# Kernel tuning notes

Measured on AMD Instinct MI355X. Metric: run time of the kernel, lower is better.

Reference implementation:

```python
import jax, jax.numpy as jnp
import numpy as np

B, S, TEXT_DIM, VISION_DIM, HIDDEN, HEADS = 4, 2048, 768, 768, 512, 8
HEAD_DIM = HIDDEN // HEADS


def setup_inputs() -> dict:
    key = jax.random.key(0)
    ks = jax.random.split(key, 9)
    s_in = 1.0 / np.sqrt(TEXT_DIM)
    s_h = 1.0 / np.sqrt(HIDDEN)
    return {
        "text_embeds": jax.random.normal(ks[0], (B, S, TEXT_DIM), dtype=jnp.float32),
        "Wq": jax.random.uniform(ks[1], (TEXT_DIM, HIDDEN), jnp.float32, -s_in, s_in),
        "bq": jax.random.uniform(ks[2], (HIDDEN,), jnp.float32, -s_in, s_in),
        "Wk": jax.random.uniform(ks[3], (TEXT_DIM, HIDDEN), jnp.float32, -s_in, s_in),
        "bk": jax.random.uniform(ks[4], (HIDDEN,), jnp.float32, -s_in, s_in),
        "Wv": jax.random.uniform(ks[5], (TEXT_DIM, HIDDEN), jnp.float32, -s_in, s_in),
        "bv": jax.random.uniform(ks[6], (HIDDEN,), jnp.float32, -s_in, s_in),
        "Wo": jax.random.uniform(ks[7], (HIDDEN, VISION_DIM), jnp.float32, -s_h, s_h),
        "bo": jax.random.uniform(ks[8], (VISION_DIM,), jnp.float32, -s_h, s_h),
    }


def reference(text_embeds, Wq, bq, Wk, bk, Wv, bv, Wo, bo):
    b, s, _ = text_embeds.shape
    # QKV projections -> [b, heads, s, head_dim]
    def proj(W, bias):
        y = jnp.einsum("bsd,dh->bsh", text_embeds, W) + bias
        return y.reshape(b, s, HEADS, HEAD_DIM).transpose(0, 2, 1, 3)
    q, k, v = proj(Wq, bq), proj(Wk, bk), proj(Wv, bv)
    scores = jnp.einsum("bhqd,bhkd->bhqk", q, k) / np.sqrt(HEAD_DIM).astype(np.float32)
    weights = jax.nn.softmax(scores, axis=-1)
    attended = jnp.einsum("bhqk,bhkd->bhqd", weights, v)
    attended = attended.transpose(0, 2, 1, 3).reshape(b, s, HIDDEN)
    out = jnp.einsum("bsh,hv->bsv", attended, Wo) + bo
    return jnp.squeeze(out, axis=1) if out.shape[1] == 1 else out
```

## Files before the change

kernel.cpp:

```cpp
#include <hip/hip_runtime.h>
#include <hip/hip_bf16.h>

#define BATCH 4
#define SEQ 2048
#define TDIM 768
#define VDIM 768
#define HID 512
#define NHEADS 8
#define HDIM 64
#define MROWS (BATCH * SEQ)
#define NQKV (3 * HID)

typedef unsigned short ushort_t;
typedef __attribute__((ext_vector_type(8))) short short8;
typedef __attribute__((ext_vector_type(4))) short short4v;
typedef __attribute__((ext_vector_type(4))) float floatx4;

#define QSCALE 0.18033688011112042f

__device__ __forceinline__ ushort_t bf16_rne(float f) {
    unsigned int u = __float_as_uint(f);
    u = (u + 0x7fffu + ((u >> 16) & 1u)) >> 16;
    return (ushort_t)u;
}

__device__ __forceinline__ float bf16_to_f(ushort_t v) {
    return __uint_as_float(((unsigned)v) << 16);
}

__device__ __forceinline__ void async16(const ushort_t* g, ushort_t* l) {
    __builtin_amdgcn_global_load_lds(
        (const __attribute__((address_space(1))) unsigned int*)g,
        (__attribute__((address_space(3))) unsigned int*)l, 16, 0, 0);
}

__global__ __launch_bounds__(256) void conv_x(const float* __restrict__ X,
                                              ushort_t* __restrict__ Xb)
{
    const int i = (blockIdx.x * 256 + threadIdx.x) * 4;
    const floatx4 v = *(const floatx4*)(X + i);
    short4v o;
#pragma unroll
    for (int j = 0; j < 4; ++j) o[j] = (short)bf16_rne(v[j]);
    *(short4v*)(Xb + i) = o;
}

__global__ __launch_bounds__(256) void transp_w(
    const float* __restrict__ Wq, const float* __restrict__ Wk,
    const float* __restrict__ Wv, const float* __restrict__ Wo,
    ushort_t* __restrict__ Wqkvt, ushort_t* __restrict__ Wot)
{
    __shared__ float tile[32][33];
    const int z = blockIdx.z;
    const float* src;
    ushort_t* dst;
    int R, C;
    if (z < 3) {
        src = (z == 0) ? Wq : (z == 1) ? Wk : Wv;
        dst = Wqkvt + (size_t)z * HID * TDIM;
        R = TDIM; C = HID;
    } else {
        src = Wo; dst = Wot; R = HID; C = VDIM;
    }
    const int tx = threadIdx.x & 31, ty = threadIdx.x >> 5;
    const int c0 = blockIdx.x * 32, r0 = blockIdx.y * 32;
    if (c0 >= C || r0 >= R) return;
#pragma unroll
    for (int i = 0; i < 4; ++i)
        tile[ty + i * 8][tx] = src[(size_t)(r0 + ty + i * 8) * C + c0 + tx];
    __syncthreads();
#pragma unroll
    for (int i = 0; i < 4; ++i)
        dst[(size_t)(c0 + ty + i * 8) * R + r0 + tx] = bf16_rne(tile[tx][ty + i * 8]);
}

template<int KD, bool SWAPPED>
__device__ __forceinline__ void gemm128(
    const ushort_t* __restrict__ A, const ushort_t* __restrict__ Bt,
    int m0, int n0, ushort_t* As, ushort_t* Bs, floatx4 (&acc)[4][4])
{
    const int tid  = threadIdx.x;
    const int lane = tid & 63;
    const int w    = tid >> 6;
    const int l15  = lane & 15;
    const int quad = lane >> 4;
    const int wrow = w >> 1;
    const int wcol = w & 1;

    const int srow = lane >> 3;
    const int scol = (lane & 7) * 8;

    const ushort_t* ga = A  + (size_t)(m0 + w * 32 + srow) * KD + scol;
    const ushort_t* gb = Bt + (size_t)(n0 + w * 32 + srow) * KD + scol;
    ushort_t* la = As + (w * 32) * 64;
    ushort_t* lb = Bs + (w * 32) * 64;

    for (int kt = 0; kt < KD; kt += 64) {
#pragma unroll
        for (int i = 0; i < 4; ++i) {
            async16(ga + (size_t)(i * 8) * KD + kt, la + i * 8 * 64);
            async16(gb + (size_t)(i * 8) * KD + kt, lb + i * 8 * 64);
        }
        __syncthreads();
#pragma unroll
        for (int half = 0; half < 2; ++half) {
            const int kk = half * 32 + quad * 8;
            short8 af[4], bf[4];
#pragma unroll
            for (int t = 0; t < 4; ++t) {
                af[t] = *(const short8*)&As[(wrow * 64 + t * 16 + l15) * 64 + kk];
                bf[t] = *(const short8*)&Bs[(wcol * 64 + t * 16 + l15) * 64 + kk];
            }
#pragma unroll
            for (int mi = 0; mi < 4; ++mi)
#pragma unroll
                for (int ni = 0; ni < 4; ++ni) {
                    if (SWAPPED)
                        acc[mi][ni] = __builtin_amdgcn_mfma_f32_16x16x32_bf16(
                            bf[ni], af[mi], acc[mi][ni], 0, 0, 0);
                    else
                        acc[mi][ni] = __builtin_amdgcn_mfma_f32_16x16x32_bf16(
                            af[mi], bf[ni], acc[mi][ni], 0, 0, 0);
                }
        }
        __syncthreads();
    }
}

__global__ __launch_bounds__(256) void qkv_gemm_mfma(
    const ushort_t* __restrict__ Xb, const ushort_t* __restrict__ Wt,
    const float* __restrict__ bq, const float* __restrict__ bk,
    const float* __restrict__ bv,
    ushort_t* __restrict__ Q, ushort_t* __restrict__ K, ushort_t* __restrict__ V)
{
    __shared__ __align__(16) ushort_t As[128 * 64];
    __shared__ __align__(16) ushort_t Bs[128 * 64];

    const int bx = blockIdx.x;
    const int m0 = blockIdx.y * 128;
    const int n0 = bx * 128;
    const int which = bx >> 2;
    const bool isV = (which == 2);

    floatx4 acc[4][4];
#pragma unroll
    for (int i = 0; i < 4; ++i)
#pragma unroll
        for (int j = 0; j < 4; ++j) acc[i][j] = (floatx4)0.0f;

    if (isV) gemm128<TDIM, false>(Xb, Wt, m0, n0, As, Bs, acc);
    else     gemm128<TDIM, true >(Xb, Wt, m0, n0, As, Bs, acc);

    const int lane = threadIdx.x & 63;
    const int w    = threadIdx.x >> 6;
    const int l15  = lane & 15;
    const int quad = lane >> 4;
    const int wrow = w >> 1;
    const int wcol = w & 1;

    if (!isV) {
        const float* bias = (which == 0) ? bq : bk;
        const float scale = (which == 0) ? QSCALE : 1.0f;
        ushort_t* Out = (which == 0) ? Q : K;
#pragma unroll
        for (int mi = 0; mi < 4; ++mi) {
            const int m = m0 + wrow * 64 + mi * 16 + l15;
            const int b = m >> 11;
            const int s = m & 2047;
#pragma unroll
            for (int ni = 0; ni < 4; ++ni) {
                const int c = (n0 - which * HID) + wcol * 64 + ni * 16 + quad * 4;
                const int h = c >> 6;
                const int d0 = c & 63;
                const floatx4 b4 = *(const floatx4*)(bias + c);
                short4v pk;
#pragma unroll
                for (int r = 0; r < 4; ++r)
                    pk[r] = (short)bf16_rne((acc[mi][ni][r] + b4[r]) * scale);
                *(short4v*)&Out[((size_t)(b * NHEADS + h) * SEQ + s) * HDIM + d0] = pk;
            }
        }
    } else {
#pragma unroll
        for (int ni = 0; ni < 4; ++ni) {
            const int c = (n0 - 2 * HID) + wcol * 64 + ni * 16 + l15;
            const int h = c >> 6;
            const int d = c & 63;
            const float b1 = bv[c];
#pragma unroll
            for (int mi = 0; mi < 4; ++mi) {
                const int mb = m0 + wrow * 64 + mi * 16 + quad * 4;
                const int b = mb >> 11;
                const int s0 = mb & 2047;
                short4v pk;
#pragma unroll
                for (int r = 0; r < 4; ++r)
                    pk[r] = (short)bf16_rne(acc[mi][ni][r] + b1);
                *(short4v*)&V[((size_t)(b * NHEADS + h) * HDIM + d) * SEQ + s0] = pk;
            }
        }
    }
}

__global__ __launch_bounds__(512) void flash_attn_mfma(
    const ushort_t* __restrict__ Q, const ushort_t* __restrict__ K,
    const ushort_t* __restrict__ Vt, ushort_t* __restrict__ Opart,
    float* __restrict__ Lpart)
{
    __shared__ __align__(16) ushort_t lds[32768];

    const int tid  = threadIdx.x;
    const int lane = tid & 63;
    const int w    = tid >> 6;
    const int l15  = lane & 15;
    const int quad = lane >> 4;
    const int key  = l15 & 7;

    const int bh = blockIdx.x;
    const int b  = bh >> 3;
    const int h  = bh & 7;
    const int q0 = blockIdx.y * 256;
    const int z  = blockIdx.z;
    const int kk0 = z * (SEQ / 2);

    const ushort_t* Qb = Q  + (size_t)bh * SEQ * HDIM;
    const ushort_t* Kb = K  + (size_t)bh * SEQ * HDIM + (size_t)kk0 * HDIM;
    const ushort_t* Vb = Vt + (size_t)bh * HDIM * SEQ + kk0;

    short8 qfA0, qfA1, qfB0, qfB1;
    {
        const ushort_t* qa = Qb + (size_t)(q0 + w * 32 + l15) * HDIM + quad * 8;
        qfA0 = *(const short8*)(qa);
        qfA1 = *(const short8*)(qa + 32);
        qfB0 = *(const short8*)(qa + 16 * HDIM);
        qfB1 = *(const short8*)(qa + 16 * HDIM + 32);
    }

    float lA = 0.f, lB = 0.f;
    floatx4 ofA[4], ofB[4];
#pragma unroll
    for (int t = 0; t < 4; ++t) { ofA[t] = (floatx4)0.0f; ofB[t] = (floatx4)0.0f; }

    const int srow = tid >> 3;
    const int sg   = tid & 7;
    const ushort_t* gK = Kb + (size_t)srow * HDIM + sg * 8;
    const ushort_t* gV = Vb + (size_t)srow * SEQ + sg * 8;
    const int sofs = srow * 64 + (sg ^ (srow & 7)) * 8;

    ushort_t* Pw = lds + 16384 + w * 2048;

    short8 kr = *(const short8*)(gK);
    short8 vr = *(const short8*)(gV);

    for (int it = 0; it < 16; ++it) {
        const int buf = it & 1;
        *(short8*)&lds[buf * 4096 + sofs]        = kr;
        *(short8*)&lds[8192 + buf * 4096 + sofs] = vr;
        __syncthreads();

        if (it < 15) {
            kr = *(const short8*)(gK + (size_t)(it + 1) * 64 * HDIM);
            vr = *(const short8*)(gV + (it + 1) * 64);
        }

        floatx4 saccA[4], saccB[4];
#pragma unroll
        for (int t = 0; t < 4; ++t) {
            const int kb = buf * 4096 + (t * 16 + l15) * 64;
            const short8 kf0 = *(const short8*)&lds[kb + (quad ^ key) * 8];
            const short8 kf1 = *(const short8*)&lds[kb + ((quad + 4) ^ key) * 8];
            floatx4 a = (floatx4)0.0f, bb = (floatx4)0.0f;
            a  = __builtin_amdgcn_mfma_f32_16x16x32_bf16(kf0, qfA0, a, 0, 0, 0);
            a  = __builtin_amdgcn_mfma_f32_16x16x32_bf16(kf1, qfA1, a, 0, 0, 0);
            bb = __builtin_amdgcn_mfma_f32_16x16x32_bf16(kf0, qfB0, bb, 0, 0, 0);
            bb = __builtin_amdgcn_mfma_f32_16x16x32_bf16(kf1, qfB1, bb, 0, 0, 0);
            saccA[t] = a;
            saccB[t] = bb;
        }

        float rsA = 0.f, rsB = 0.f;
#pragma unroll
        for (int t = 0; t < 4; ++t) {
            float pa[4], pb[4];
#pragma unroll
            for (int r = 0; r < 4; ++r) {
                pa[r] = exp2f(saccA[t][r]); rsA += pa[r];
                pb[r] = exp2f(saccB[t][r]); rsB += pb[r];
            }
            const int pofs = ((2 * t + (quad >> 1)) ^ key) * 8 + (quad & 1) * 4;
            {
                const unsigned u0 = __float_as_uint(pa[0]) + 0x8000u;
                const unsigned u1 = __float_as_uint(pa[1]) + 0x8000u;
                const unsigned u2 = __float_as_uint(pa[2]) + 0x8000u;
                const unsigned u3 = __float_as_uint(pa[3]) + 0x8000u;
                const unsigned lo = __builtin_amdgcn_perm(u1, u0, 0x07060302u);
                const unsigned hi = __builtin_amdgcn_perm(u3, u2, 0x07060302u);
                *(unsigned long long*)&Pw[l15 * 64 + pofs] =
                    ((unsigned long long)hi << 32) | lo;
            }
            {
                const unsigned u0 = __float_as_uint(pb[0]) + 0x8000u;
                const unsigned u1 = __float_as_uint(pb[1]) + 0x8000u;
                const unsigned u2 = __float_as_uint(pb[2]) + 0x8000u;
                const unsigned u3 = __float_as_uint(pb[3]) + 0x8000u;
                const unsigned lo = __builtin_amdgcn_perm(u1, u0, 0x07060302u);
                const unsigned hi = __builtin_amdgcn_perm(u3, u2, 0x07060302u);
                *(unsigned long long*)&Pw[(16 + l15) * 64 + pofs] =
                    ((unsigned long long)hi << 32) | lo;
            }
        }
        lA += rsA;
        lB += rsB;
        asm volatile("s_waitcnt lgkmcnt(0)" ::: "memory");

        const short8 pfA0 = *(const short8*)&Pw[l15 * 64 + (quad ^ key) * 8];
        const short8 pfA1 = *(const short8*)&Pw[l15 * 64 + ((quad + 4) ^ key) * 8];
        const short8 pfB0 = *(const short8*)&Pw[(16 + l15) * 64 + (quad ^ key) * 8];
        const short8 pfB1 = *(const short8*)&Pw[(16 + l15) * 64 + ((quad + 4) ^ key) * 8];

#pragma unroll
        for (int t = 0; t < 4; ++t) {
            const int vb2 = 8192 + buf * 4096 + (t * 16 + l15) * 64;
            const short8 vf0 = *(const short8*)&lds[vb2 + (quad ^ key) * 8];
            const short8 vf1 = *(const short8*)&lds[vb2 + ((quad + 4) ^ key) * 8];
            ofA[t] = __builtin_amdgcn_mfma_f32_16x16x32_bf16(vf0, pfA0, ofA[t], 0, 0, 0);
            ofA[t] = __builtin_amdgcn_mfma_f32_16x16x32_bf16(vf1, pfA1, ofA[t], 0, 0, 0);
            ofB[t] = __builtin_amdgcn_mfma_f32_16x16x32_bf16(vf0, pfB0, ofB[t], 0, 0, 0);
            ofB[t] = __builtin_amdgcn_mfma_f32_16x16x32_bf16(vf1, pfB1, ofB[t], 0, 0, 0);
        }
    }

    lA += __shfl_xor(lA, 16); lA += __shfl_xor(lA, 32);
    lB += __shfl_xor(lB, 16); lB += __shfl_xor(lB, 32);

    const int sA = q0 + w * 32 + l15;
    ushort_t* arowA = Opart + (size_t)z * MROWS * HID
                    + ((size_t)(b * SEQ + sA)) * HID + h * HDIM;
    ushort_t* arowB = arowA + (size_t)16 * HID;
#pragma unroll
    for (int t = 0; t < 4; ++t) {
        short4v pkA, pkB;
#pragma unroll
        for (int r = 0; r < 4; ++r) {
            pkA[r] = (short)bf16_rne(ofA[t][r]);
            pkB[r] = (short)bf16_rne(ofB[t][r]);
        }
        *(short4v*)&arowA[t * 16 + quad * 4] = pkA;
        *(short4v*)&arowB[t * 16 + quad * 4] = pkB;
    }
    if (quad == 0) {
        Lpart[(size_t)(z * 32 + bh) * SEQ + sA]      = lA;
        Lpart[(size_t)(z * 32 + bh) * SEQ + sA + 16] = lB;
    }
}

__global__ __launch_bounds__(256) void combine_halves(
    const ushort_t* __restrict__ Opart, const float* __restrict__ Lpart,
    ushort_t* __restrict__ Att)
{
    const int idx = blockIdx.x * 256 + threadIdx.x;
    const int m  = idx >> 6;
    const int c0 = (idx & 63) * 8;
    const int b = m >> 11;
    const int s = m & 2047;
    const int h = c0 >> 6;
    const int bh = b * 8 + h;

    const float l = Lpart[(size_t)bh * SEQ + s] +
                    Lpart[(size_t)(32 + bh) * SEQ + s];
    const float inv = 1.f / l;

    const short8 o0 = *(const short8*)&Opart[(size_t)m * HID + c0];
    const short8 o1 = *(const short8*)&Opart[(size_t)MROWS * HID + (size_t)m * HID + c0];
    short8 o;
#pragma unroll
    for (int j = 0; j < 8; ++j) {
        const float f = (bf16_to_f((ushort_t)o0[j]) + bf16_to_f((ushort_t)o1[j])) * inv;
        o[j] = (short)bf16_rne(f);
    }
    *(short8*)&Att[(size_t)m * HID + c0] = o;
}

__global__ __launch_bounds__(256) void out_gemm_mfma(
    const ushort_t* __restrict__ Attb, const ushort_t* __restrict__ Wot,
    const float* __restrict__ bo, float* __restrict__ Y)
{
    __shared__ __align__(16) ushort_t As[128 * 64];
    __shared__ __align__(16) ushort_t Bs[128 * 64];

    const int m0 = blockIdx.y * 128;
    const int n0 = blockIdx.x * 128;

    floatx4 acc[4][4];
#pragma unroll
    for (int i = 0; i < 4; ++i)
#pragma unroll
        for (int j = 0; j < 4; ++j) acc[i][j] = (floatx4)0.0f;

    gemm128<HID, true>(Attb, Wot, m0, n0, As, Bs, acc);

    const int lane = threadIdx.x & 63;
    const int w    = threadIdx.x >> 6;
    const int l15  = lane & 15;
    const int quad = lane >> 4;
    const int wrow = w >> 1;
    const int wcol = w & 1;

#pragma unroll
    for (int mi = 0; mi < 4; ++mi) {
        const int m = m0 + wrow * 64 + mi * 16 + l15;
#pragma unroll
        for (int ni = 0; ni < 4; ++ni) {
            const int nb = n0 + wcol * 64 + ni * 16 + quad * 4;
            const floatx4 b4 = *(const floatx4*)(bo + nb);
            floatx4 o;
#pragma unroll
            for (int r = 0; r < 4; ++r) o[r] = acc[mi][ni][r] + b4[r];
            *(floatx4*)&Y[(size_t)m * VDIM + nb] = o;
        }
    }
}

extern "C" void kernel_launch(void* const* d_in, const int* in_sizes, int n_in,
                              void* d_out, int out_size, void* d_ws, size_t ws_size,
                              hipStream_t stream)
{
    const float* text = (const float*)d_in[0];
    const float* Wq = (const float*)d_in[1];
    const float* bq = (const float*)d_in[2];
    const float* Wk = (const float*)d_in[3];
    const float* bk = (const float*)d_in[4];
    const float* Wv = (const float*)d_in[5];
    const float* bv = (const float*)d_in[6];
    const float* Wo = (const float*)d_in[7];
    const float* bo = (const float*)d_in[8];
    float* out = (float*)d_out;

    ushort_t* Xb    = (ushort_t*)d_ws;
    ushort_t* Wqkvt = Xb + (size_t)MROWS * TDIM;
    ushort_t* Wot   = Wqkvt + (size_t)NQKV * TDIM;
    ushort_t* Qw    = Wot + (size_t)VDIM * HID;
    ushort_t* Kw    = Qw + (size_t)MROWS * HID;
    ushort_t* Vtw   = Kw + (size_t)MROWS * HID;
    ushort_t* Opart = Vtw + (size_t)MROWS * HID;
    float*    Lpart = (float*)(Opart + (size_t)2 * MROWS * HID);
    ushort_t* Attb  = Xb;

    conv_x<<<dim3(MROWS * TDIM / 1024), 256, 0, stream>>>(text, Xb);
    transp_w<<<dim3(24, 24, 4), 256, 0, stream>>>(Wq, Wk, Wv, Wo, Wqkvt, Wot);
    qkv_gemm_mfma<<<dim3(12, 64), 256, 0, stream>>>(Xb, Wqkvt, bq, bk, bv, Qw, Kw, Vtw);
    flash_attn_mfma<<<dim3(32, 8, 2), 512, 0, stream>>>(Qw, Kw, Vtw, Opart, Lpart);
    combine_halves<<<dim3(MROWS * HID / 8 / 256), 256, 0, stream>>>(Opart, Lpart, Attb);
    out_gemm_mfma<<<dim3(6, 64), 256, 0, stream>>>(Attb, Wot, bo, out);
}
```

Before: 214.4 us.

## Fuse split-KV combine into output projection GEMM and merge prep kernels

Merges the input conversion and weight transpose into one prep launch, and folds the split-attention combine (sum of two partial outputs divided by the summed softmax denominators) into the A-tile load of a new output-projection GEMM using 128x64 tiles. This removes two kernel launches and the write and reread of the intermediate attention buffer. In exchange, each of the 12 column blocks re-reads both partial outputs and recomputes the normalisation. The new GEMM loads synchronously with no async pipelining and rounds with a simpler add-0x8000 scheme.

```diff
diff --git a/kernel.cpp b/kernel.cpp
--- a/kernel.cpp
+++ b/kernel.cpp
@@ -15,6 +15,7 @@
 typedef __attribute__((ext_vector_type(8))) short short8;
 typedef __attribute__((ext_vector_type(4))) short short4v;
 typedef __attribute__((ext_vector_type(4))) float floatx4;
+typedef __attribute__((ext_vector_type(4))) unsigned int uint4v;
 
 #define QSCALE 0.18033688011112042f
 
@@ -34,24 +35,29 @@
         (__attribute__((address_space(3))) unsigned int*)l, 16, 0, 0);
 }
 
-__global__ __launch_bounds__(256) void conv_x(const float* __restrict__ X,
-                                              ushort_t* __restrict__ Xb)
-{
-    const int i = (blockIdx.x * 256 + threadIdx.x) * 4;
-    const floatx4 v = *(const floatx4*)(X + i);
-    short4v o;
-#pragma unroll
-    for (int j = 0; j < 4; ++j) o[j] = (short)bf16_rne(v[j]);
-    *(short4v*)(Xb + i) = o;
-}
-
-__global__ __launch_bounds__(256) void transp_w(
+__global__ __launch_bounds__(256) void prep(
+    const float* __restrict__ X, ushort_t* __restrict__ Xb,
     const float* __restrict__ Wq, const float* __restrict__ Wk,
     const float* __restrict__ Wv, const float* __restrict__ Wo,
     ushort_t* __restrict__ Wqkvt, ushort_t* __restrict__ Wot)
 {
     __shared__ float tile[32][33];
-    const int z = blockIdx.z;
+    const int bx = blockIdx.x;
+    if (bx < 6144) {
+        const int i = (bx * 256 + threadIdx.x) * 4;
+        const floatx4 v = *(const floatx4*)(X + i);
+        short4v o;
+#pragma unroll
+        for (int j = 0; j < 4; ++j) o[j] = (short)bf16_rne(v[j]);
+        *(short4v*)(Xb + i) = o;
+        return;
+    }
+    const int t = bx - 6144;
+    const int z = t / 576;
+    const int rem = t % 576;
+    const int bxx = rem % 24;
+    const int byy = rem / 24;
+
     const float* src;
     ushort_t* dst;
     int R, C;
@@ -63,7 +69,7 @@
         src = Wo; dst = Wot; R = HID; C = VDIM;
     }
     const int tx = threadIdx.x & 31, ty = threadIdx.x >> 5;
-    const int c0 = blockIdx.x * 32, r0 = blockIdx.y * 32;
+    const int c0 = bxx * 32, r0 = byy * 32;
     if (c0 >= C || r0 >= R) return;
 #pragma unroll
     for (int i = 0; i < 4; ++i)
@@ -354,68 +360,108 @@
     }
 }
 
-__global__ __launch_bounds__(256) void combine_halves(
+__global__ __launch_bounds__(256) void out_proj_fused(
     const ushort_t* __restrict__ Opart, const float* __restrict__ Lpart,
-    ushort_t* __restrict__ Att)
-{
-    const int idx = blockIdx.x * 256 + threadIdx.x;
-    const int m  = idx >> 6;
-    const int c0 = (idx & 63) * 8;
-    const int b = m >> 11;
-    const int s = m & 2047;
-    const int h = c0 >> 6;
-    const int bh = b * 8 + h;
-
-    const float l = Lpart[(size_t)bh * SEQ + s] +
-                    Lpart[(size_t)(32 + bh) * SEQ + s];
-    const float inv = 1.f / l;
-
-    const short8 o0 = *(const short8*)&Opart[(size_t)m * HID + c0];
-    const short8 o1 = *(const short8*)&Opart[(size_t)MROWS * HID + (size_t)m * HID + c0];
-    short8 o;
-#pragma unroll
-    for (int j = 0; j < 8; ++j) {
-        const float f = (bf16_to_f((ushort_t)o0[j]) + bf16_to_f((ushort_t)o1[j])) * inv;
-        o[j] = (short)bf16_rne(f);
-    }
-    *(short8*)&Att[(size_t)m * HID + c0] = o;
-}
-
-__global__ __launch_bounds__(256) void out_gemm_mfma(
-    const ushort_t* __restrict__ Attb, const ushort_t* __restrict__ Wot,
-    const float* __restrict__ bo, float* __restrict__ Y)
+    const ushort_t* __restrict__ Wot, const float* __restrict__ bo,
+    float* __restrict__ Y)
 {
     __shared__ __align__(16) ushort_t As[128 * 64];
-    __shared__ __align__(16) ushort_t Bs[128 * 64];
-
-    const int m0 = blockIdx.y * 128;
-    const int n0 = blockIdx.x * 128;
-
-    floatx4 acc[4][4];
-#pragma unroll
-    for (int i = 0; i < 4; ++i)
-#pragma unroll
-        for (int j = 0; j < 4; ++j) acc[i][j] = (floatx4)0.0f;
-
-    gemm128<HID, true>(Attb, Wot, m0, n0, As, Bs, acc);
-
-    const int lane = threadIdx.x & 63;
-    const int w    = threadIdx.x >> 6;
+    __shared__ __align__(16) ushort_t Bs[64 * 64];
+
+    const int tid  = threadIdx.x;
+    const int lane = tid & 63;
+    const int w    = tid >> 6;
     const int l15  = lane & 15;
     const int quad = lane >> 4;
-    const int wrow = w >> 1;
-    const int wcol = w & 1;
-
-#pragma unroll
-    for (int mi = 0; mi < 4; ++mi) {
-        const int m = m0 + wrow * 64 + mi * 16 + l15;
-#pragma unroll
-        for (int ni = 0; ni < 4; ++ni) {
-            const int nb = n0 + wcol * 64 + ni * 16 + quad * 4;
+    const int key  = l15 & 7;
+
+    const int n0 = blockIdx.x * 64;
+    const int m0 = blockIdx.y * 128;
+
+    const int srow = tid >> 1;
+    const int scol = (tid & 1) * 32;
+    const int am   = m0 + srow;
+    const int ab   = am >> 11;
+    const int as   = am & 2047;
+    const ushort_t* gO0 = Opart + (size_t)am * HID + scol;
+    const ushort_t* gO1 = gO0 + (size_t)MROWS * HID;
+    const int sk = srow & 7;
+
+    const int brow = tid >> 3;
+    const int bg   = tid & 7;
+    const ushort_t* gB = Wot + (size_t)(n0 + brow) * HID + bg * 8;
+
+    floatx4 acc[2][4];
+#pragma unroll
+    for (int i = 0; i < 2; ++i)
+#pragma unroll
+        for (int j = 0; j < 4; ++j) acc[i][j] = (floatx4)0.0f;
+
+    for (int kt = 0; kt < HID; kt += 64) {
+        const int h = kt >> 6;
+        const int bh = ab * 8 + h;
+        const float l = Lpart[(size_t)bh * SEQ + as] +
+                        Lpart[(size_t)(32 + bh) * SEQ + as];
+        const float inv = 1.f / l;
+        if (kt) __syncthreads();
+#pragma unroll
+        for (int seg = 0; seg < 4; ++seg) {
+            const short8 o0 = *(const short8*)(gO0 + h * 64 + seg * 8);
+            const short8 o1 = *(const short8*)(gO1 + h * 64 + seg * 8);
+            uint4v v;
+#pragma unroll
+            for (int p = 0; p < 4; ++p) {
+                const float f0 = (bf16_to_f((ushort_t)o0[2 * p]) +
+                                  bf16_to_f((ushort_t)o1[2 * p])) * inv;
+                const float f1 = (bf16_to_f((ushort_t)o0[2 * p + 1]) +
+                                  bf16_to_f((ushort_t)o1[2 * p + 1])) * inv;
+                const unsigned u0 = __float_as_uint(f0) + 0x8000u;
+                const unsigned u1 = __float_as_uint(f1) + 0x8000u;
+                v[p] = __builtin_amdgcn_perm(u1, u0, 0x07060302u);
+            }
+            const int g = (scol >> 3) + seg;
+            *(uint4v*)&As[srow * 64 + (g ^ sk) * 8] = v;
+        }
+        {
+            const short8 b0 = *(const short8*)(gB + kt);
+            const short8 b1 = *(const short8*)(gB + (size_t)32 * HID + kt);
+            *(short8*)&Bs[brow * 64 + (bg ^ (brow & 7)) * 8] = b0;
+            *(short8*)&Bs[(brow + 32) * 64 + (bg ^ (brow & 7)) * 8] = b1;
+        }
+        __syncthreads();
+
+#pragma unroll
+        for (int half = 0; half < 2; ++half) {
+            short8 af[2], bf[4];
+#pragma unroll
+            for (int t = 0; t < 2; ++t) {
+                const int row = w * 32 + t * 16 + l15;
+                af[t] = *(const short8*)&As[row * 64 + (((half * 4) + quad) ^ key) * 8];
+            }
+#pragma unroll
+            for (int n = 0; n < 4; ++n) {
+                const int row = n * 16 + l15;
+                bf[n] = *(const short8*)&Bs[row * 64 + (((half * 4) + quad) ^ key) * 8];
+            }
+#pragma unroll
+            for (int t = 0; t < 2; ++t)
+#pragma unroll
+                for (int n = 0; n < 4; ++n)
+                    acc[t][n] = __builtin_amdgcn_mfma_f32_16x16x32_bf16(
+                        bf[n], af[t], acc[t][n], 0, 0, 0);
+        }
+    }
+
+#pragma unroll
+    for (int t = 0; t < 2; ++t) {
+        const int m = m0 + w * 32 + t * 16 + l15;
+#pragma unroll
+        for (int n = 0; n < 4; ++n) {
+            const int nb = n0 + n * 16 + quad * 4;
             const floatx4 b4 = *(const floatx4*)(bo + nb);
             floatx4 o;
 #pragma unroll
-            for (int r = 0; r < 4; ++r) o[r] = acc[mi][ni][r] + b4[r];
+            for (int r = 0; r < 4; ++r) o[r] = acc[t][n][r] + b4[r];
             *(floatx4*)&Y[(size_t)m * VDIM + nb] = o;
         }
     }
@@ -444,12 +490,9 @@
     ushort_t* Vtw   = Kw + (size_t)MROWS * HID;
     ushort_t* Opart = Vtw + (size_t)MROWS * HID;
     float*    Lpart = (float*)(Opart + (size_t)2 * MROWS * HID);
-    ushort_t* Attb  = Xb;
-
-    conv_x<<<dim3(MROWS * TDIM / 1024), 256, 0, stream>>>(text, Xb);
-    transp_w<<<dim3(24, 24, 4), 256, 0, stream>>>(Wq, Wk, Wv, Wo, Wqkvt, Wot);
+
+    prep<<<dim3(8448), 256, 0, stream>>>(text, Xb, Wq, Wk, Wv, Wo, Wqkvt, Wot);
     qkv_gemm_mfma<<<dim3(12, 64), 256, 0, stream>>>(Xb, Wqkvt, bq, bk, bv, Qw, Kw, Vtw);
     flash_attn_mfma<<<dim3(32, 8, 2), 512, 0, stream>>>(Qw, Kw, Vtw, Opart, Lpart);
-    combine_halves<<<dim3(MROWS * HID / 8 / 256), 256, 0, stream>>>(Opart, Lpart, Attb);
-    out_gemm_mfma<<<dim3(6, 64), 256, 0, stream>>>(Attb, Wot, bo, out);
-}
+    out_proj_fused<<<dim3(12, 64), 256, 0, stream>>>(Opart, Lpart, Wot, bo, out);
+}
```

Measured after the change: 222.4 us. 3.7% more time.
